# Kernel tuning notes

Measured on AMD Instinct MI355X. Metric: run time of the kernel, lower is better.

Reference implementation:

```python
import jax, jax.numpy as jnp
import numpy as np

TEMPERATURE = 0.07
MARGIN = 0.15
HARD_NEG_RATIO = 0.5


def setup_inputs() -> dict:
    key = jax.random.key(0)
    k1, k2, k3 = jax.random.split(key, 3)
    B, D = 4096, 128
    drug_emb = jax.random.normal(k1, (B, D), dtype=jnp.float32)
    se_emb = jax.random.normal(k2, (B, D), dtype=jnp.float32)
    # labels spread over [0, 5) so that |diff| > 1.0 negatives exist
    labels = jax.random.uniform(k3, (B,), dtype=jnp.float32) * 5.0
    return {"drug_emb": drug_emb, "se_emb": se_emb, "labels": labels}


def _single_branch_loss(z, labels):
    B = z.shape[0]
    # F.normalize(z, dim=-1): divide by norm clamped to eps
    z = z / jnp.maximum(jnp.linalg.norm(z, axis=-1, keepdims=True), 1e-12)
    sim = jnp.matmul(z, z.T) / TEMPERATURE                      # [B, B]
    label_diff = jnp.abs(labels[None, :] - labels[:, None])     # [B, B]
    self_mask = ~jnp.eye(B, dtype=bool)
    pos_weight = jnp.exp(-label_diff / MARGIN) * self_mask      # soft positives
    neg_mask = (label_diff > 1.0) & self_mask

    # k = max(int(mean per-row negative count * ratio), 1), capped at B-1
    mean_negs = jnp.mean(jnp.sum(neg_mask.astype(jnp.float32), axis=1))
    k = jnp.maximum((mean_negs * HARD_NEG_RATIO).astype(jnp.int32), 1)
    k = jnp.minimum(k, B - 1)

    sim_max = jax.lax.stop_gradient(jnp.max(sim, axis=1, keepdims=True))
    logits = sim - sim_max

    # hard-negative top-k per row, as a static-shape rank test (jit-safe)
    neg_sim = jnp.where(neg_mask, sim, -jnp.inf)
    ranks = jnp.argsort(jnp.argsort(-neg_sim, axis=1), axis=1)  # 0 = largest
    hard_neg_mask = (ranks < k) & neg_mask

    any_neg = jnp.any(neg_mask)
    denom_mask = jnp.where(any_neg, hard_neg_mask | (pos_weight > 0.1), self_mask)

    exp_denom = jnp.sum(jnp.exp(logits) * denom_mask, axis=1, keepdims=True) + 1e-8
    log_prob = logits - jnp.log(exp_denom)
    weighted_log_prob = jnp.sum(pos_weight * log_prob, axis=1)
    denom = jnp.maximum(jnp.sum(pos_weight, axis=1), 1e-8)
    return -jnp.mean(weighted_log_prob / denom)


def reference(drug_emb, se_emb, labels):
    loss_drug = _single_branch_loss(drug_emb, labels)
    loss_se = _single_branch_loss(se_emb, labels)
    loss_cross = _single_branch_loss(drug_emb * se_emb, labels)
    return (loss_drug + loss_se + loss_cross) / 3.0
```

## Files before the change

kernel.cpp:

```cpp
#include <hip/hip_runtime.h>
#include <math.h>

#define BB 4096
#define DD 128

typedef __attribute__((ext_vector_type(8))) short bf16x8;
typedef __attribute__((ext_vector_type(4))) float f32x4;

__device__ __forceinline__ unsigned fkey(float x){
    unsigned b = __float_as_uint(x);
    return (b & 0x80000000u) ? ~b : (b | 0x80000000u);
}
__device__ __forceinline__ float funkey(unsigned u){
    unsigned b = (u & 0x80000000u) ? (u & 0x7fffffffu) : ~u;
    return __uint_as_float(b);
}

__device__ __forceinline__ float blkSumF(float v, volatile float* sh){
    #pragma unroll
    for (int o = 32; o > 0; o >>= 1) v += __shfl_down(v, o);
    int t = threadIdx.x;
    __syncthreads();
    if ((t & 63) == 0) sh[t >> 6] = v;
    __syncthreads();
    return (sh[0] + sh[1]) + (sh[2] + sh[3]);
}
__device__ __forceinline__ float blkMaxF(float v, volatile float* sh){
    #pragma unroll
    for (int o = 32; o > 0; o >>= 1) v = fmaxf(v, __shfl_down(v, o));
    int t = threadIdx.x;
    __syncthreads();
    if ((t & 63) == 0) sh[t >> 6] = v;
    __syncthreads();
    return fmaxf(fmaxf(sh[0], sh[1]), fmaxf(sh[2], sh[3]));
}
__device__ __forceinline__ int blkSumI(int v, volatile int* sh){
    #pragma unroll
    for (int o = 32; o > 0; o >>= 1) v += __shfl_down(v, o);
    int t = threadIdx.x;
    __syncthreads();
    if ((t & 63) == 0) sh[t >> 6] = v;
    __syncthreads();
    return (sh[0] + sh[1]) + (sh[2] + sh[3]);
}

__global__ void krn_normalize(const float* __restrict__ drug, const float* __restrict__ se,
                              ushort* __restrict__ Z){
    int row = blockIdx.x, br = blockIdx.y, t = threadIdx.x;
    float dv = drug[row * DD + t];
    float sv = se[row * DD + t];
    float v = (br == 0) ? dv : ((br == 1) ? sv : dv * sv);
    float sq = v * v;
    #pragma unroll
    for (int o = 32; o > 0; o >>= 1) sq += __shfl_down(sq, o);
    __shared__ float sh[2];
    if ((t & 63) == 0) sh[t >> 6] = sq;
    __syncthreads();
    float nrm = sqrtf(sh[0] + sh[1]);
    float outv = v / fmaxf(nrm, 1e-12f);
    unsigned u = __float_as_uint(outv);
    unsigned r = (u + 0x7FFFu + ((u >> 16) & 1u)) >> 16;
    int col = t ^ ((row & 7) << 3);
    Z[((size_t)br * BB + row) * DD + col] = (ushort)r;
}

__global__ void krn_init(int* __restrict__ ntot){ *ntot = 0; }

__global__ __launch_bounds__(256) void krn_negcount(const float* __restrict__ labels,
                                                    int* __restrict__ ntot){
    __shared__ float lab[BB];
    __shared__ int shi[4];
    int t = threadIdx.x;
    #pragma unroll
    for (int e = 0; e < 4; ++e)
        ((float4*)lab)[t + e * 256] = ((const float4*)labels)[t + e * 256];
    __syncthreads();
    int i0 = blockIdx.x * 16;
    int c = 0;
    for (int ii = 0; ii < 16; ++ii){
        float li = lab[i0 + ii];
        #pragma unroll
        for (int e = 0; e < 16; ++e){
            int j = t + e * 256;
            c += (fabsf(li - lab[j]) > 1.0f) ? 1 : 0;
        }
    }
    int cc = blkSumI(c, shi);
    if (t == 0) atomicAdd(ntot, cc);
}

__global__ void krn_calck(const int* __restrict__ ntot, int* __restrict__ kflags){
    int N = *ntot;
    int k = N >> 13;
    if (k < 1) k = 1;
    if (k > BB - 1) k = BB - 1;
    kflags[0] = k;
    kflags[1] = (N > 0) ? 1 : 0;
}

__device__ __forceinline__ bf16x8 frag_ld(const ushort* base, int row, int e0){
    int e = e0 ^ ((row & 7) << 3);
    return *(const bf16x8*)(base + row * DD + e);
}

__global__ __launch_bounds__(256) void krn_gemm(const ushort* __restrict__ Zb,
                                                float* __restrict__ sim, int r0){
    __shared__ ushort As[128 * DD];
    __shared__ ushort Bs[128 * DD];
    int t = threadIdx.x;
    int rowbase = r0 + blockIdx.y * 128;
    int colbase = blockIdx.x * 128;

    {
        const float4* gA = (const float4*)(Zb + (size_t)rowbase * DD);
        const float4* gB = (const float4*)(Zb + (size_t)colbase * DD);
        float4* lA = (float4*)As;
        float4* lB = (float4*)Bs;
        #pragma unroll
        for (int it = 0; it < 8; ++it){
            lA[it * 256 + t] = gA[it * 256 + t];
            lB[it * 256 + t] = gB[it * 256 + t];
        }
    }
    __syncthreads();

    int wid = t >> 6, lane = t & 63;
    int wr = (wid >> 1) * 64, wc = (wid & 1) * 64;
    int fr = lane & 15, fq = lane >> 4;

    f32x4 acc[4][4];
    #pragma unroll
    for (int m = 0; m < 4; ++m)
        #pragma unroll
        for (int n = 0; n < 4; ++n)
            acc[m][n] = (f32x4){0.f, 0.f, 0.f, 0.f};

    #pragma unroll
    for (int ks = 0; ks < 4; ++ks){
        int e0 = ks * 32 + fq * 8;
        bf16x8 a0 = frag_ld(As, wr + 0 * 16 + fr, e0);
        bf16x8 a1 = frag_ld(As, wr + 1 * 16 + fr, e0);
        bf16x8 a2 = frag_ld(As, wr + 2 * 16 + fr, e0);
        bf16x8 a3 = frag_ld(As, wr + 3 * 16 + fr, e0);
        bf16x8 b0 = frag_ld(Bs, wc + 0 * 16 + fr, e0);
        bf16x8 b1 = frag_ld(Bs, wc + 1 * 16 + fr, e0);
        bf16x8 b2 = frag_ld(Bs, wc + 2 * 16 + fr, e0);
        bf16x8 b3 = frag_ld(Bs, wc + 3 * 16 + fr, e0);
        acc[0][0] = __builtin_amdgcn_mfma_f32_16x16x32_bf16(a0, b0, acc[0][0], 0, 0, 0);
        acc[0][1] = __builtin_amdgcn_mfma_f32_16x16x32_bf16(a0, b1, acc[0][1], 0, 0, 0);
        acc[0][2] = __builtin_amdgcn_mfma_f32_16x16x32_bf16(a0, b2, acc[0][2], 0, 0, 0);
        acc[0][3] = __builtin_amdgcn_mfma_f32_16x16x32_bf16(a0, b3, acc[0][3], 0, 0, 0);
        acc[1][0] = __builtin_amdgcn_mfma_f32_16x16x32_bf16(a1, b0, acc[1][0], 0, 0, 0);
        acc[1][1] = __builtin_amdgcn_mfma_f32_16x16x32_bf16(a1, b1, acc[1][1], 0, 0, 0);
        acc[1][2] = __builtin_amdgcn_mfma_f32_16x16x32_bf16(a1, b2, acc[1][2], 0, 0, 0);
        acc[1][3] = __builtin_amdgcn_mfma_f32_16x16x32_bf16(a1, b3, acc[1][3], 0, 0, 0);
        acc[2][0] = __builtin_amdgcn_mfma_f32_16x16x32_bf16(a2, b0, acc[2][0], 0, 0, 0);
        acc[2][1] = __builtin_amdgcn_mfma_f32_16x16x32_bf16(a2, b1, acc[2][1], 0, 0, 0);
        acc[2][2] = __builtin_amdgcn_mfma_f32_16x16x32_bf16(a2, b2, acc[2][2], 0, 0, 0);
        acc[2][3] = __builtin_amdgcn_mfma_f32_16x16x32_bf16(a2, b3, acc[2][3], 0, 0, 0);
        acc[3][0] = __builtin_amdgcn_mfma_f32_16x16x32_bf16(a3, b0, acc[3][0], 0, 0, 0);
        acc[3][1] = __builtin_amdgcn_mfma_f32_16x16x32_bf16(a3, b1, acc[3][1], 0, 0, 0);
        acc[3][2] = __builtin_amdgcn_mfma_f32_16x16x32_bf16(a3, b2, acc[3][2], 0, 0, 0);
        acc[3][3] = __builtin_amdgcn_mfma_f32_16x16x32_bf16(a3, b3, acc[3][3], 0, 0, 0);
    }

    const float invT = 1.0f / 0.07f;
    int srow0 = blockIdx.y * 128 + wr + fq * 4;
    int scol0 = colbase + wc + fr;
    #pragma unroll
    for (int m = 0; m < 4; ++m){
        #pragma unroll
        for (int n = 0; n < 4; ++n){
            f32x4 c = acc[m][n];
            #pragma unroll
            for (int j = 0; j < 4; ++j)
                sim[(size_t)(srow0 + m * 16 + j) * BB + scol0 + n * 16] = c[j] * invT;
        }
    }
}

__global__ __launch_bounds__(256) void krn_stats(const float* __restrict__ sim,
                                                 const float* __restrict__ labels,
                                                 const int* __restrict__ kflags,
                                                 float* __restrict__ rowloss, int r0){
    __shared__ int hist[256];
    __shared__ int wsum[4];
    __shared__ float redf[4];
    __shared__ int redi[4];
    __shared__ unsigned selb[2];

    int t = threadIdx.x;
    int i = r0 + blockIdx.x;
    float li = labels[i];

    hist[t] = 0;
    __syncthreads();

    float s[16];
    unsigned negbits = 0, posbits = 0, selfbits = 0;
    float m = -INFINITY, pwsum = 0.f, pwsim = 0.f;
    int ncnt = 0;

    const float4* srow4 = (const float4*)(sim + (size_t)blockIdx.x * BB);
    const float4* lab4  = (const float4*)labels;

    #pragma unroll
    for (int e = 0; e < 4; ++e){
        float4 sv = srow4[t + e * 256];
        float4 lv = lab4[t + e * 256];
        int jbase = (t + e * 256) * 4;
        float ss[4] = {sv.x, sv.y, sv.z, sv.w};
        float ll[4] = {lv.x, lv.y, lv.z, lv.w};
        #pragma unroll
        for (int c = 0; c < 4; ++c){
            int idx = e * 4 + c;
            float val = ss[c];
            s[idx] = val;
            m = fmaxf(m, val);
            float d = fabsf(li - ll[c]);
            int j = jbase + c;
            if (d > 1.0f){
                negbits |= 1u << idx;
                ncnt++;
                atomicAdd(&hist[fkey(val) >> 24], 1);
            }
            if (j == i){
                selfbits |= 1u << idx;
            } else {
                float pw = __expf(d * (-1.0f / 0.15f));
                pwsum += pw;
                pwsim += pw * val;
                if (d < 0.34538776f) posbits |= 1u << idx;
            }
        }
    }

    float M     = blkMaxF(m, redf);
    float PWS   = blkSumF(pwsum, redf);
    float PWSIM = blkSumF(pwsim, redf);
    int   NC    = blkSumI(ncnt, redi);

    int kk = kflags[0];
    int anyneg = kflags[1];
    int mode = anyneg ? ((NC <= kk) ? 1 : 0) : 2;
    unsigned ukth = 0;
    int r = kk;

    if (mode == 0){
        unsigned prefix = 0;
        for (int level = 3; level >= 0; --level){
            int shl = level * 8;
            if (level < 3){
                hist[t] = 0;
                __syncthreads();
                #pragma unroll
                for (int idx = 0; idx < 16; ++idx){
                    if (negbits & (1u << idx)){
                        unsigned u = fkey(s[idx]);
                        if ((u >> (shl + 8)) == prefix)
                            atomicAdd(&hist[(u >> shl) & 255u], 1);
                    }
                }
                __syncthreads();
            }
            int b = 255 - t;
            int hv = hist[b];
            int v = hv;
            #pragma unroll
            for (int o = 1; o < 64; o <<= 1){
                int u2 = __shfl_up(v, o);
                if ((t & 63) >= o) v += u2;
            }
            if ((t & 63) == 63) wsum[t >> 6] = v;
            __syncthreads();
            int w = t >> 6;
            int pre = (w > 0 ? wsum[0] : 0) + (w > 1 ? wsum[1] : 0) + (w > 2 ? wsum[2] : 0);
            v += pre;
            int above_excl = v - hv;
            if (above_excl < r && r <= v){
                selb[0] = (unsigned)b;
                selb[1] = (unsigned)above_excl;
            }
            __syncthreads();
            prefix = (prefix << 8) | selb[0];
            r -= (int)selb[1];
            __syncthreads();
        }
        ukth = prefix;
    }

    float El = 0.f;
    unsigned em;
    if (mode == 2)      em = 0xFFFFu & ~selfbits;
    else if (mode == 1) em = negbits | posbits;
    else                em = posbits;
    #pragma unroll
    for (int idx = 0; idx < 16; ++idx)
        if (em & (1u << idx)) El += __expf(s[idx] - M);
    if (mode == 0){
        #pragma unroll
        for (int idx = 0; idx < 16; ++idx)
            if ((negbits & (1u << idx)) && fkey(s[idx]) > ukth)
                El += __expf(s[idx] - M);
    }
    float Etot = blkSumF(El, redf);

    if (t == 0){
        if (mode == 0) Etot += (float)r * __expf(funkey(ukth) - M);
        float logE = __logf(Etot + 1e-8f);
        float w  = (PWSIM - M * PWS) - PWS * logE;
        float dn = fmaxf(PWS, 1e-8f);
        rowloss[i] = w / dn;
    }
}

__global__ void krn_final(const float* __restrict__ rowloss, float* __restrict__ out){
    __shared__ float redf[4];
    int t = threadIdx.x;
    float total = 0.f;
    for (int b = 0; b < 3; ++b){
        float ssum = 0.f;
        for (int e = 0; e < 16; ++e) ssum += rowloss[b * BB + t + e * 256];
        float S = blkSumF(ssum, redf);
        total += S * (1.0f / BB);
    }
    if (t == 0) out[0] = -total / 3.0f;
}

extern "C" void kernel_launch(void* const* d_in, const int* in_sizes, int n_in,
                              void* d_out, int out_size, void* d_ws, size_t ws_size,
                              hipStream_t stream){
    const float* drug   = (const float*)d_in[0];
    const float* se     = (const float*)d_in[1];
    const float* labels = (const float*)d_in[2];
    float* out = (float*)d_out;
    char* ws = (char*)d_ws;

    const size_t zbytes = (size_t)3 * BB * DD * sizeof(ushort);
    const size_t tail   = (size_t)3 * BB * sizeof(float) + 256;

    int slab = BB;
    while (slab > 128 && zbytes + tail + (size_t)slab * BB * sizeof(float) > ws_size)
        slab >>= 1;

    ushort* Z      = (ushort*)ws;
    float* simbuf  = (float*)(ws + zbytes);
    size_t off     = zbytes + (size_t)slab * BB * sizeof(float);
    float* rowloss = (float*)(ws + off);  off += (size_t)3 * BB * sizeof(float);
    int*   ntot    = (int*)(ws + off);
    int*   kflags  = ntot + 2;

    krn_normalize<<<dim3(BB, 3), 128, 0, stream>>>(drug, se, Z);
    krn_init<<<1, 1, 0, stream>>>(ntot);
    krn_negcount<<<256, 256, 0, stream>>>(labels, ntot);
    krn_calck<<<1, 1, 0, stream>>>(ntot, kflags);

    int nslab = BB / slab;
    for (int b = 0; b < 3; ++b){
        const ushort* Zb = Z + (size_t)b * BB * DD;
        for (int s2 = 0; s2 < nslab; ++s2){
            krn_gemm<<<dim3(BB / 128, slab / 128), 256, 0, stream>>>(Zb, simbuf, s2 * slab);
            krn_stats<<<slab, 256, 0, stream>>>(simbuf, labels, kflags, rowloss + b * BB, s2 * slab);
        }
    }
    krn_final<<<1, 256, 0, stream>>>(rowloss, out);
}
```

Before: 208.3 us.

## Batch three branches into one GEMM/stats launch and replace radix select with adaptive bucketing

```diff
diff --git a/kernel.cpp b/kernel.cpp
--- a/kernel.cpp
+++ b/kernel.cpp
@@ -8,8 +8,8 @@
 typedef __attribute__((ext_vector_type(4))) float f32x4;
 
 __device__ __forceinline__ unsigned fkey(float x){
-    unsigned b = __float_as_uint(x);
-    return (b & 0x80000000u) ? ~b : (b | 0x80000000u);
+    int b = __float_as_int(x);
+    return (unsigned)(b ^ ((b >> 31) | 0x80000000));
 }
 __device__ __forceinline__ float funkey(unsigned u){
     unsigned b = (u & 0x80000000u) ? (u & 0x7fffffffu) : ~u;
@@ -103,10 +103,13 @@
     return *(const bf16x8*)(base + row * DD + e);
 }
 
-__global__ __launch_bounds__(256) void krn_gemm(const ushort* __restrict__ Zb,
-                                                float* __restrict__ sim, int r0){
+__global__ __launch_bounds__(256) void krn_gemm(const ushort* __restrict__ Z,
+                                                float* __restrict__ sim, size_t simStride,
+                                                int r0){
     __shared__ ushort As[128 * DD];
     __shared__ ushort Bs[128 * DD];
+    const ushort* Zb = Z + (size_t)blockIdx.z * (BB * DD);
+    float* simz = sim + (size_t)blockIdx.z * simStride;
     int t = threadIdx.x;
     int rowbase = r0 + blockIdx.y * 128;
     int colbase = blockIdx.x * 128;
@@ -174,144 +177,211 @@
             f32x4 c = acc[m][n];
             #pragma unroll
             for (int j = 0; j < 4; ++j)
-                sim[(size_t)(srow0 + m * 16 + j) * BB + scol0 + n * 16] = c[j] * invT;
-        }
-    }
-}
-
-__global__ __launch_bounds__(256) void krn_stats(const float* __restrict__ sim,
-                                                 const float* __restrict__ labels,
-                                                 const int* __restrict__ kflags,
-                                                 float* __restrict__ rowloss, int r0){
-    __shared__ int hist[256];
-    __shared__ int wsum[4];
-    __shared__ float redf[4];
-    __shared__ int redi[4];
-    __shared__ unsigned selb[2];
-
-    int t = threadIdx.x;
-    int i = r0 + blockIdx.x;
-    float li = labels[i];
-
-    hist[t] = 0;
-    __syncthreads();
-
-    float s[16];
-    unsigned negbits = 0, posbits = 0, selfbits = 0;
-    float m = -INFINITY, pwsum = 0.f, pwsim = 0.f;
-    int ncnt = 0;
-
-    const float4* srow4 = (const float4*)(sim + (size_t)blockIdx.x * BB);
-    const float4* lab4  = (const float4*)labels;
-
-    #pragma unroll
-    for (int e = 0; e < 4; ++e){
-        float4 sv = srow4[t + e * 256];
-        float4 lv = lab4[t + e * 256];
-        int jbase = (t + e * 256) * 4;
-        float ss[4] = {sv.x, sv.y, sv.z, sv.w};
-        float ll[4] = {lv.x, lv.y, lv.z, lv.w};
-        #pragma unroll
-        for (int c = 0; c < 4; ++c){
-            int idx = e * 4 + c;
-            float val = ss[c];
-            s[idx] = val;
-            m = fmaxf(m, val);
-            float d = fabsf(li - ll[c]);
-            int j = jbase + c;
-            if (d > 1.0f){
-                negbits |= 1u << idx;
-                ncnt++;
-                atomicAdd(&hist[fkey(val) >> 24], 1);
+                simz[(size_t)(srow0 + m * 16 + j) * BB + scol0 + n * 16] = c[j] * invT;
+        }
+    }
+}
+
+__device__ __forceinline__ void branch_tail(
+    const float (&s)[16], float Mb, float psimb, float PWS,
+    int mode, int kk, unsigned negbits, unsigned posbits, unsigned selfbits,
+    int t, int bi, int i, float* __restrict__ rowloss,
+    int* hist, int* wsum, volatile float* redf,
+    volatile unsigned* selb, volatile unsigned* sel2, int* cnt, unsigned* list)
+{
+    unsigned ukth = 0;
+    int rfin = 0;
+
+    if (mode == 0){
+        unsigned klo = 0x3E7FFFFFu;
+        unsigned khi = 0xC1800000u;
+        int rp = kk;
+        while (true){
+            if (klo == khi){ ukth = klo; rfin = rp; break; }
+            unsigned range = khi - klo;
+            int sh = 22 - __clz(range);
+            if (sh < 0) sh = 0;
+            hist[t] = 0; hist[t + 256] = 0; hist[t + 512] = 0; hist[t + 768] = 0;
+            __syncthreads();
+            #pragma unroll
+            for (int idx = 0; idx < 16; ++idx){
+                if (negbits & (1u << idx)){
+                    unsigned u = fkey(s[idx]);
+                    if (u >= klo && u <= khi)
+                        atomicAdd(&hist[(u - klo) >> sh], 1);
+                }
             }
-            if (j == i){
-                selfbits |= 1u << idx;
-            } else {
-                float pw = __expf(d * (-1.0f / 0.15f));
-                pwsum += pw;
-                pwsim += pw * val;
-                if (d < 0.34538776f) posbits |= 1u << idx;
+            __syncthreads();
+            {
+                int g = 255 - t;
+                int h0 = hist[4*g], h1 = hist[4*g+1], h2 = hist[4*g+2], h3 = hist[4*g+3];
+                int Sg = h0 + h1 + h2 + h3;
+                int v = Sg;
+                #pragma unroll
+                for (int o = 1; o < 64; o <<= 1){
+                    int u2 = __shfl_up(v, o);
+                    if ((t & 63) >= o) v += u2;
+                }
+                if ((t & 63) == 63) wsum[t >> 6] = v;
+                __syncthreads();
+                int w = t >> 6;
+                int pre = (w > 0 ? wsum[0] : 0) + (w > 1 ? wsum[1] : 0) + (w > 2 ? wsum[2] : 0);
+                v += pre;
+                int ge = v - Sg;
+                int a3 = ge + h3, a2 = a3 + h2, a1 = a2 + h1, a0 = a1 + h0;
+                if (a0 - h0 < rp && rp <= a0){ selb[0] = 4u*g+0u; selb[1] = (unsigned)(a0-h0); selb[2] = (unsigned)h0; }
+                if (a1 - h1 < rp && rp <= a1){ selb[0] = 4u*g+1u; selb[1] = (unsigned)(a1-h1); selb[2] = (unsigned)h1; }
+                if (a2 - h2 < rp && rp <= a2){ selb[0] = 4u*g+2u; selb[1] = (unsigned)(a2-h2); selb[2] = (unsigned)h2; }
+                if (a3 - h3 < rp && rp <= a3){ selb[0] = 4u*g+3u; selb[1] = (unsigned)(a3-h3); selb[2] = (unsigned)h3; }
             }
-        }
-    }
-
-    float M     = blkMaxF(m, redf);
-    float PWS   = blkSumF(pwsum, redf);
-    float PWSIM = blkSumF(pwsim, redf);
-    int   NC    = blkSumI(ncnt, redi);
-
-    int kk = kflags[0];
-    int anyneg = kflags[1];
-    int mode = anyneg ? ((NC <= kk) ? 1 : 0) : 2;
-    unsigned ukth = 0;
-    int r = kk;
-
-    if (mode == 0){
-        unsigned prefix = 0;
-        for (int level = 3; level >= 0; --level){
-            int shl = level * 8;
-            if (level < 3){
-                hist[t] = 0;
+            __syncthreads();
+            unsigned B = selb[0];
+            int ae = (int)selb[1];
+            int c  = (int)selb[2];
+            rp -= ae;
+            klo = klo + (B << sh);
+            unsigned nhi = klo + ((1u << sh) - 1u);
+            if (nhi < khi) khi = nhi;
+            if (c <= 48){
+                if (t == 0) *cnt = 0;
                 __syncthreads();
                 #pragma unroll
                 for (int idx = 0; idx < 16; ++idx){
                     if (negbits & (1u << idx)){
                         unsigned u = fkey(s[idx]);
-                        if ((u >> (shl + 8)) == prefix)
-                            atomicAdd(&hist[(u >> shl) & 255u], 1);
+                        if (u >= klo && u <= khi){
+                            int p = atomicAdd(cnt, 1);
+                            list[p] = u;
+                        }
                     }
                 }
                 __syncthreads();
-            }
-            int b = 255 - t;
-            int hv = hist[b];
-            int v = hv;
-            #pragma unroll
-            for (int o = 1; o < 64; o <<= 1){
-                int u2 = __shfl_up(v, o);
-                if ((t & 63) >= o) v += u2;
-            }
-            if ((t & 63) == 63) wsum[t >> 6] = v;
-            __syncthreads();
-            int w = t >> 6;
-            int pre = (w > 0 ? wsum[0] : 0) + (w > 1 ? wsum[1] : 0) + (w > 2 ? wsum[2] : 0);
-            v += pre;
-            int above_excl = v - hv;
-            if (above_excl < r && r <= v){
-                selb[0] = (unsigned)b;
-                selb[1] = (unsigned)above_excl;
+                int cc = *cnt;
+                if (t < cc){
+                    unsigned kj = list[t];
+                    int g2 = 0, e2 = 0;
+                    for (int mm = 0; mm < cc; ++mm){
+                        unsigned km = list[mm];
+                        g2 += (km > kj) ? 1 : 0;
+                        e2 += (km == kj) ? 1 : 0;
+                    }
+                    if (g2 < rp && rp <= g2 + e2){ sel2[0] = kj; sel2[1] = (unsigned)g2; }
+                }
+                __syncthreads();
+                ukth = sel2[0];
+                rfin = rp - (int)sel2[1];
+                break;
             }
             __syncthreads();
-            prefix = (prefix << 8) | selb[0];
-            r -= (int)selb[1];
-            __syncthreads();
-        }
-        ukth = prefix;
+        }
     }
 
     float El = 0.f;
-    unsigned em;
-    if (mode == 2)      em = 0xFFFFu & ~selfbits;
-    else if (mode == 1) em = negbits | posbits;
-    else                em = posbits;
-    #pragma unroll
-    for (int idx = 0; idx < 16; ++idx)
-        if (em & (1u << idx)) El += __expf(s[idx] - M);
-    if (mode == 0){
+    if (mode == 2){
         #pragma unroll
         for (int idx = 0; idx < 16; ++idx)
-            if ((negbits & (1u << idx)) && fkey(s[idx]) > ukth)
-                El += __expf(s[idx] - M);
+            if (!(selfbits & (1u << idx))) El += __expf(s[idx] - Mb);
+    } else if (mode == 1){
+        unsigned em = negbits | posbits;
+        #pragma unroll
+        for (int idx = 0; idx < 16; ++idx)
+            if (em & (1u << idx)) El += __expf(s[idx] - Mb);
+    } else {
+        #pragma unroll
+        for (int idx = 0; idx < 16; ++idx){
+            unsigned bit = 1u << idx;
+            bool dm = (posbits & bit) != 0u;
+            if (negbits & bit) dm = dm || (fkey(s[idx]) > ukth);
+            if (dm) El += __expf(s[idx] - Mb);
+        }
     }
     float Etot = blkSumF(El, redf);
 
     if (t == 0){
-        if (mode == 0) Etot += (float)r * __expf(funkey(ukth) - M);
+        if (mode == 0) Etot += (float)rfin * __expf(funkey(ukth) - Mb);
         float logE = __logf(Etot + 1e-8f);
-        float w  = (PWSIM - M * PWS) - PWS * logE;
-        float dn = fmaxf(PWS, 1e-8f);
-        rowloss[i] = w / dn;
-    }
+        float w = (psimb - Mb * PWS) - PWS * logE;
+        rowloss[bi * BB + i] = w / fmaxf(PWS, 1e-8f);
+    }
+}
+
+__global__ __launch_bounds__(256) void krn_stats(const float* __restrict__ sim, size_t simStride,
+                                                 const float* __restrict__ labels,
+                                                 const int* __restrict__ kflags,
+                                                 float* __restrict__ rowloss, int r0){
+    __shared__ int hist[1024];
+    __shared__ int wsum[4];
+    __shared__ float redf[4];
+    __shared__ int redi[4];
+    __shared__ unsigned selb[3];
+    __shared__ unsigned sel2[2];
+    __shared__ int cnt;
+    __shared__ unsigned list[64];
+
+    int t = threadIdx.x;
+    int i = r0 + blockIdx.x;
+    float li = labels[i];
+
+    float s0[16], s1[16], s2[16];
+    unsigned negbits = 0, posbits = 0, selfbits = 0;
+    float m0 = -INFINITY, m1 = -INFINITY, m2 = -INFINITY;
+    float pws = 0.f, ps0 = 0.f, ps1 = 0.f, ps2 = 0.f;
+    int ncnt = 0;
+
+    const float4* r0p = (const float4*)(sim + (size_t)blockIdx.x * BB);
+    const float4* r1p = (const float4*)(sim + simStride + (size_t)blockIdx.x * BB);
+    const float4* r2p = (const float4*)(sim + 2 * simStride + (size_t)blockIdx.x * BB);
+    const float4* lab4 = (const float4*)labels;
+
+    #pragma unroll
+    for (int e = 0; e < 4; ++e){
+        float4 v0 = r0p[t + e * 256];
+        float4 v1 = r1p[t + e * 256];
+        float4 v2 = r2p[t + e * 256];
+        float4 lv = lab4[t + e * 256];
+        float a0c[4] = {v0.x, v0.y, v0.z, v0.w};
+        float a1c[4] = {v1.x, v1.y, v1.z, v1.w};
+        float a2c[4] = {v2.x, v2.y, v2.z, v2.w};
+        float llc[4] = {lv.x, lv.y, lv.z, lv.w};
+        int jbase = (t + e * 256) * 4;
+        #pragma unroll
+        for (int c = 0; c < 4; ++c){
+            int idx = e * 4 + c;
+            float sv0 = a0c[c], sv1 = a1c[c], sv2 = a2c[c];
+            s0[idx] = sv0; s1[idx] = sv1; s2[idx] = sv2;
+            m0 = fmaxf(m0, sv0); m1 = fmaxf(m1, sv1); m2 = fmaxf(m2, sv2);
+            float d = fabsf(li - llc[c]);
+            int j = jbase + c;
+            bool self = (j == i);
+            if (self) selfbits |= 1u << idx;
+            if (d > 1.0f){ negbits |= 1u << idx; ncnt++; }
+            else if (!self && d < 0.34538776f) posbits |= 1u << idx;
+            if (!self){
+                float pw = __expf(d * (-1.0f / 0.15f));
+                pws += pw;
+                ps0 += pw * sv0; ps1 += pw * sv1; ps2 += pw * sv2;
+            }
+        }
+    }
+
+    float M0 = blkMaxF(m0, redf);
+    float M1 = blkMaxF(m1, redf);
+    float M2 = blkMaxF(m2, redf);
+    float P0 = blkSumF(ps0, redf);
+    float P1 = blkSumF(ps1, redf);
+    float P2 = blkSumF(ps2, redf);
+    float PWS = blkSumF(pws, redf);
+    int NC = blkSumI(ncnt, redi);
+
+    int kk = kflags[0], anyneg = kflags[1];
+    int mode = anyneg ? ((NC <= kk) ? 1 : 0) : 2;
+
+    branch_tail(s0, M0, P0, PWS, mode, kk, negbits, posbits, selfbits,
+                t, 0, i, rowloss, hist, wsum, redf, selb, sel2, &cnt, list);
+    branch_tail(s1, M1, P1, PWS, mode, kk, negbits, posbits, selfbits,
+                t, 1, i, rowloss, hist, wsum, redf, selb, sel2, &cnt, list);
+    branch_tail(s2, M2, P2, PWS, mode, kk, negbits, posbits, selfbits,
+                t, 2, i, rowloss, hist, wsum, redf, selb, sel2, &cnt, list);
 }
 
 __global__ void krn_final(const float* __restrict__ rowloss, float* __restrict__ out){
@@ -340,12 +410,13 @@
     const size_t tail   = (size_t)3 * BB * sizeof(float) + 256;
 
     int slab = BB;
-    while (slab > 128 && zbytes + tail + (size_t)slab * BB * sizeof(float) > ws_size)
+    while (slab > 128 && zbytes + tail + (size_t)3 * slab * BB * sizeof(float) > ws_size)
         slab >>= 1;
+    size_t simStride = (size_t)slab * BB;
 
     ushort* Z      = (ushort*)ws;
     float* simbuf  = (float*)(ws + zbytes);
-    size_t off     = zbytes + (size_t)slab * BB * sizeof(float);
+    size_t off     = zbytes + (size_t)3 * simStride * sizeof(float);
     float* rowloss = (float*)(ws + off);  off += (size_t)3 * BB * sizeof(float);
     int*   ntot    = (int*)(ws + off);
     int*   kflags  = ntot + 2;
@@ -356,12 +427,9 @@
     krn_calck<<<1, 1, 0, stream>>>(ntot, kflags);
 
     int nslab = BB / slab;
-    for (int b = 0; b < 3; ++b){
-        const ushort* Zb = Z + (size_t)b * BB * DD;
-        for (int s2 = 0; s2 < nslab; ++s2){
-            krn_gemm<<<dim3(BB / 128, slab / 128), 256, 0, stream>>>(Zb, simbuf, s2 * slab);
-            krn_stats<<<slab, 256, 0, stream>>>(simbuf, labels, kflags, rowloss + b * BB, s2 * slab);
-        }
+    for (int s2 = 0; s2 < nslab; ++s2){
+        krn_gemm<<<dim3(BB / 128, slab / 128, 3), 256, 0, stream>>>(Z, simbuf, simStride, s2 * slab);
+        krn_stats<<<slab, 256, 0, stream>>>(simbuf, simStride, labels, kflags, rowloss, s2 * slab);
     }
     krn_final<<<1, 256, 0, stream>>>(rowloss, out);
 }
```

New measurement: 217.6 us. 4.5% more time.
